# Kernel tuning notes

Measured on AMD Instinct MI355X. Metric: run time of the kernel, lower is better.

Reference implementation:

```python
import jax, jax.numpy as jnp
import numpy as np

N_NODES = 10000
N_EDGES = 640000
D_FEAT = 128


def setup_inputs() -> dict:
    key = jax.random.key(0)
    k1, k2, k3, k4 = jax.random.split(key, 4)
    feat = jax.random.normal(k1, (N_NODES, D_FEAT), dtype=jnp.float32)
    src = jax.random.randint(k2, (N_EDGES,), 0, N_NODES, dtype=jnp.int32)
    dst = jax.random.randint(k3, (N_EDGES,), 0, N_NODES, dtype=jnp.int32)
    W = jax.random.normal(k4, (D_FEAT, D_FEAT), dtype=jnp.float32) / np.sqrt(D_FEAT).astype(np.float32)
    b = jnp.zeros((D_FEAT,), dtype=jnp.float32)
    return {"feat": feat, "W": W, "b": b, "src": src, "dst": dst}


def reference(feat, W, b, src, dst):
    eps = jnp.float32(0.0)  # init_eps=0, learn_eps=False (buffer)
    n = feat.shape[0]
    # message passing: copy_u('h','m') + sum reducer -> neigh[i] = sum_{j->i} h_j
    h_src = feat[src]                                   # [E, D] gather
    neigh = jax.ops.segment_sum(h_src, dst, num_segments=n)  # [N, D] scatter-add
    rst = (1.0 + eps) * feat + neigh
    # apply_func: Linear(D, D)
    rst = rst @ W + b
    # per-edge score: e = sum(h_src * tanh(h_dst), axis=1)
    e = jnp.sum(h_src * jnp.tanh(feat[dst]), axis=1)    # [E]
    # edge_softmax: softmax over edges grouped by destination node
    m = jax.ops.segment_max(e, dst, num_segments=n)     # [N]
    e_exp = jnp.exp(e - m[dst])
    denom = jax.ops.segment_sum(e_exp, dst, num_segments=n)  # [N]
    e_soft = e_exp / denom[dst]
    return rst, e_soft
```

## Files before the change

### kernel.cpp

```cpp
#include <hip/hip_runtime.h>
#include <hip/hip_bf16.h>
#include <math.h>

#define N_NODES 10000
#define N_EDGES 640000
#define D_FEAT  128
#define SLOT    128


__global__ void scatter_build(const int* __restrict__ src,
                              const int* __restrict__ dst,
                              int* __restrict__ cnt,
                              unsigned short* __restrict__ slot_us,
                              int* __restrict__ pos_by_edge) {
    int i = blockIdx.x * 256 + threadIdx.x;
    int d = dst[i];
    int pos = atomicAdd(&cnt[d], 1);
    int idx = d * SLOT + pos;
    slot_us[idx] = (unsigned short)src[i];
    pos_by_edge[i] = idx;
}

__global__ void fused_node(const float* __restrict__ feat,
                           const int* __restrict__ cnt,
                           const unsigned short* __restrict__ slot_us,
                           float* __restrict__ e_slot,
                           float* __restrict__ x_out) {
    __shared__ float t_sh[4][D_FEAT];
    __shared__ float e_sh[4][SLOT];
    int wv = threadIdx.x >> 6;
    int lane = threadIdx.x & 63;
    int node = blockIdx.x * 4 + wv;
    if (node >= N_NODES) return;

    int g = lane >> 4;
    int l = lane & 15;

    int deg = cnt[node];
    unsigned base = (unsigned)node * SLOT;

    float2 fd2 = ((const float2*)(feat + (size_t)node * D_FEAT))[lane];
    ((float2*)&t_sh[wv][0])[lane] = make_float2(tanhf(fd2.x), tanhf(fd2.y));
    float4 t0 = ((const float4*)&t_sh[wv][0])[l * 2];
    float4 t1 = ((const float4*)&t_sh[wv][0])[l * 2 + 1];

    float4 acc0 = make_float4(0.f, 0.f, 0.f, 0.f);
    float4 acc1 = make_float4(0.f, 0.f, 0.f, 0.f);

    for (int cbase = 0; cbase < deg; cbase += 64) {
        int n = min(64, deg - cbase);
        int my_src = (int)slot_us[base + min(cbase + lane, deg - 1)];
        int j = 0;
        for (; j + 8 <= n; j += 8) {
            int s0 = __shfl(my_src, j + g, 64);
            int s1 = __shfl(my_src, j + 4 + g, 64);
            const float4* r0 = (const float4*)(feat + (size_t)s0 * D_FEAT) + l * 2;
            const float4* r1 = (const float4*)(feat + (size_t)s1 * D_FEAT) + l * 2;
            float4 v00 = r0[0], v01 = r0[1];
            float4 v10 = r1[0], v11 = r1[1];
            acc0.x += v00.x + v10.x; acc0.y += v00.y + v10.y;
            acc0.z += v00.z + v10.z; acc0.w += v00.w + v10.w;
            acc1.x += v01.x + v11.x; acc1.y += v01.y + v11.y;
            acc1.z += v01.z + v11.z; acc1.w += v01.w + v11.w;
            float d0 = v00.x * t0.x + v00.y * t0.y + v00.z * t0.z + v00.w * t0.w
                     + v01.x * t1.x + v01.y * t1.y + v01.z * t1.z + v01.w * t1.w;
            float d1 = v10.x * t0.x + v10.y * t0.y + v10.z * t0.z + v10.w * t0.w
                     + v11.x * t1.x + v11.y * t1.y + v11.z * t1.z + v11.w * t1.w;
            #pragma unroll
            for (int off = 1; off <= 8; off <<= 1) {
                d0 += __shfl_xor(d0, off, 64);
                d1 += __shfl_xor(d1, off, 64);
            }
            if (l == 0) {
                e_sh[wv][cbase + j + g] = d0;
                e_sh[wv][cbase + j + 4 + g] = d1;
            }
        }
        for (; j < n; j += 4) {
            int idx = j + g;
            bool act = idx < n;
            int s = __shfl(my_src, min(idx, n - 1), 64);
            const float4* r0 = (const float4*)(feat + (size_t)s * D_FEAT) + l * 2;
            float4 v0 = r0[0], v1 = r0[1];
            if (!act) {
                v0 = make_float4(0.f, 0.f, 0.f, 0.f);
                v1 = make_float4(0.f, 0.f, 0.f, 0.f);
            }
            acc0.x += v0.x; acc0.y += v0.y; acc0.z += v0.z; acc0.w += v0.w;
            acc1.x += v1.x; acc1.y += v1.y; acc1.z += v1.z; acc1.w += v1.w;
            float d = v0.x * t0.x + v0.y * t0.y + v0.z * t0.z + v0.w * t0.w
                    + v1.x * t1.x + v1.y * t1.y + v1.z * t1.z + v1.w * t1.w;
            #pragma unroll
            for (int off = 1; off <= 8; off <<= 1)
                d += __shfl_xor(d, off, 64);
            if (act && l == 0) e_sh[wv][cbase + idx] = d;
        }
    }

    #pragma unroll
    for (int off = 16; off <= 32; off <<= 1) {
        acc0.x += __shfl_xor(acc0.x, off, 64);
        acc0.y += __shfl_xor(acc0.y, off, 64);
        acc0.z += __shfl_xor(acc0.z, off, 64);
        acc0.w += __shfl_xor(acc0.w, off, 64);
        acc1.x += __shfl_xor(acc1.x, off, 64);
        acc1.y += __shfl_xor(acc1.y, off, 64);
        acc1.z += __shfl_xor(acc1.z, off, 64);
        acc1.w += __shfl_xor(acc1.w, off, 64);
    }

    float2 mp = (g == 0) ? make_float2(acc0.x, acc0.y)
              : (g == 1) ? make_float2(acc0.z, acc0.w)
              : (g == 2) ? make_float2(acc1.x, acc1.y)
              :            make_float2(acc1.z, acc1.w);
    int p2 = l * 4 + g;
    float2 fn = ((const float2*)(feat + (size_t)node * D_FEAT))[p2];
    ((float2*)(x_out + (size_t)node * D_FEAT))[p2] =
        make_float2(mp.x + fn.x, mp.y + fn.y);

    float mx = -INFINITY;
    for (int i = lane; i < deg; i += 64) mx = fmaxf(mx, e_sh[wv][i]);
    #pragma unroll
    for (int off = 32; off; off >>= 1)
        mx = fmaxf(mx, __shfl_xor(mx, off, 64));

    float sum = 0.f;
    for (int i = lane; i < deg; i += 64) {
        float ex = expf(e_sh[wv][i] - mx);
        e_sh[wv][i] = ex;
        sum += ex;
    }
    #pragma unroll
    for (int off = 32; off; off >>= 1)
        sum += __shfl_xor(sum, off, 64);

    float inv = 1.0f / sum;
    for (int i = lane; i < deg; i += 64)
        e_slot[base + i] = e_sh[wv][i] * inv;
}

__global__ void gemm_and_edge(float* __restrict__ io,
                              const float* __restrict__ W,
                              const float* __restrict__ b,
                              const int* __restrict__ pos_by_edge,
                              const float* __restrict__ e_slot,
                              float* __restrict__ out_e) {
    if (blockIdx.x >= 625) {
        int i4 = ((blockIdx.x - 625) * 256 + threadIdx.x) * 4;
        int4 p = *(const int4*)&pos_by_edge[i4];
        float4 r;
        r.x = e_slot[p.x];
        r.y = e_slot[p.y];
        r.z = e_slot[p.z];
        r.w = e_slot[p.w];
        *(float4*)&out_e[i4] = r;
        return;
    }

    __shared__ float xst[D_FEAT][20];
    int rbase = blockIdx.x * 16;

    for (int i = threadIdx.x; i < 16 * D_FEAT; i += 256) {
        int r = i >> 7, c = i & 127;
        xst[c][r] = io[(size_t)(rbase + r) * D_FEAT + c];
    }
    __syncthreads();

    int col = threadIdx.x & 127;
    int rh  = threadIdx.x >> 7;
    float acc[8] = {0.f, 0.f, 0.f, 0.f, 0.f, 0.f, 0.f, 0.f};

    for (int k = 0; k < D_FEAT; ++k) {
        float4 xa = *(const float4*)&xst[k][rh * 8];
        float4 xb = *(const float4*)&xst[k][rh * 8 + 4];
        float wk = W[(size_t)k * D_FEAT + col];
        acc[0] += xa.x * wk; acc[1] += xa.y * wk;
        acc[2] += xa.z * wk; acc[3] += xa.w * wk;
        acc[4] += xb.x * wk; acc[5] += xb.y * wk;
        acc[6] += xb.z * wk; acc[7] += xb.w * wk;
    }
    __syncthreads();

    float bias = b[col];
    #pragma unroll
    for (int r = 0; r < 8; ++r)
        io[(size_t)(rbase + rh * 8 + r) * D_FEAT + col] = acc[r] + bias;
}

extern "C" void kernel_launch(void* const* d_in, const int* in_sizes, int n_in,
                              void* d_out, int out_size, void* d_ws, size_t ws_size,
                              hipStream_t stream) {
    const float* feat = (const float*)d_in[0];
    const float* W    = (const float*)d_in[1];
    const float* b    = (const float*)d_in[2];
    const int*   src  = (const int*)d_in[3];
    const int*   dst  = (const int*)d_in[4];

    float* out_rst = (float*)d_out;
    float* out_e   = (float*)d_out + (size_t)N_NODES * D_FEAT;

    char* ws = (char*)d_ws;
    int*            cnt         = (int*)(ws + 0);
    unsigned short* slot_us     = (unsigned short*)(ws + 65536);
    float*          e_slot      = (float*)(ws + 2686976);
    int*            pos_by_edge = (int*)(ws + 7806976);

    hipMemsetAsync(cnt, 0, N_NODES * sizeof(int), stream);

    scatter_build<<<N_EDGES / 256, 256, 0, stream>>>(src, dst, cnt, slot_us, pos_by_edge);

    fused_node<<<(N_NODES + 3) / 4, 256, 0, stream>>>(feat, cnt, slot_us, e_slot, out_rst);

    gemm_and_edge<<<1250, 256, 0, stream>>>(out_rst, W, b, pos_by_edge, e_slot, out_e);
}
```

Baseline: 148.2 us.

## Split per-node edge counters into 8 sub-buckets to reduce atomic contention

Each destination node now has 8 counters and 8 slot segments of 64, chosen by the block index, so atomics in scatter_build land on different addresses. fused_node prefix-sums the 8 counts, compacts the source indices into shared memory, and writes softmax results back to the segmented layout. This targets same-address atomic serialization, at the cost of a larger workspace, a memset eight times bigger, and assumptions that no segment exceeds 64 entries and no node exceeds 128 edges.

```diff
diff --git a/kernel.cpp b/kernel.cpp
--- a/kernel.cpp
+++ b/kernel.cpp
@@ -5,7 +5,9 @@
 #define N_NODES 10000
 #define N_EDGES 640000
 #define D_FEAT  128
-#define SLOT    128
+#define NGRP    8
+#define SEG     64
+#define MAXDEG  128
 
 
 __global__ void scatter_build(const int* __restrict__ src,
@@ -14,9 +16,10 @@
                               unsigned short* __restrict__ slot_us,
                               int* __restrict__ pos_by_edge) {
     int i = blockIdx.x * 256 + threadIdx.x;
+    int g = blockIdx.x & 7;
     int d = dst[i];
-    int pos = atomicAdd(&cnt[d], 1);
-    int idx = d * SLOT + pos;
+    int pos = atomicAdd(&cnt[d * NGRP + g], 1);
+    int idx = d * (NGRP * SEG) + g * SEG + pos;
     slot_us[idx] = (unsigned short)src[i];
     pos_by_edge[i] = idx;
 }
@@ -27,7 +30,8 @@
                            float* __restrict__ e_slot,
                            float* __restrict__ x_out) {
     __shared__ float t_sh[4][D_FEAT];
-    __shared__ float e_sh[4][SLOT];
+    __shared__ float e_sh[4][MAXDEG];
+    __shared__ unsigned short src_sh[4][MAXDEG];
     int wv = threadIdx.x >> 6;
     int lane = threadIdx.x & 63;
     int node = blockIdx.x * 4 + wv;
@@ -36,8 +40,22 @@
     int g = lane >> 4;
     int l = lane & 15;
 
-    int deg = cnt[node];
-    unsigned base = (unsigned)node * SLOT;
+    unsigned sbase = (unsigned)node * (NGRP * SEG);
+
+    int cme = (lane < NGRP) ? cnt[node * NGRP + lane] : 0;
+    int cg[NGRP], psum[NGRP + 1];
+    psum[0] = 0;
+    #pragma unroll
+    for (int k = 0; k < NGRP; ++k) {
+        cg[k] = __shfl(cme, k, 64);
+        psum[k + 1] = psum[k] + cg[k];
+    }
+    int deg = psum[NGRP];
+    #pragma unroll
+    for (int k = 0; k < NGRP; ++k) {
+        if (lane < cg[k])
+            src_sh[wv][psum[k] + lane] = slot_us[sbase + k * SEG + lane];
+    }
 
     float2 fd2 = ((const float2*)(feat + (size_t)node * D_FEAT))[lane];
     ((float2*)&t_sh[wv][0])[lane] = make_float2(tanhf(fd2.x), tanhf(fd2.y));
@@ -49,7 +67,7 @@
 
     for (int cbase = 0; cbase < deg; cbase += 64) {
         int n = min(64, deg - cbase);
-        int my_src = (int)slot_us[base + min(cbase + lane, deg - 1)];
+        int my_src = (int)src_sh[wv][min(cbase + lane, deg - 1)];
         int j = 0;
         for (; j + 8 <= n; j += 8) {
             int s0 = __shfl(my_src, j + g, 64);
@@ -135,8 +153,11 @@
         sum += __shfl_xor(sum, off, 64);
 
     float inv = 1.0f / sum;
-    for (int i = lane; i < deg; i += 64)
-        e_slot[base + i] = e_sh[wv][i] * inv;
+    #pragma unroll
+    for (int k = 0; k < NGRP; ++k) {
+        if (lane < cg[k])
+            e_slot[sbase + k * SEG + lane] = e_sh[wv][psum[k] + lane] * inv;
+    }
 }
 
 __global__ void gemm_and_edge(float* __restrict__ io,
@@ -201,11 +222,11 @@
 
     char* ws = (char*)d_ws;
     int*            cnt         = (int*)(ws + 0);
-    unsigned short* slot_us     = (unsigned short*)(ws + 65536);
-    float*          e_slot      = (float*)(ws + 2686976);
-    int*            pos_by_edge = (int*)(ws + 7806976);
-
-    hipMemsetAsync(cnt, 0, N_NODES * sizeof(int), stream);
+    unsigned short* slot_us     = (unsigned short*)(ws + 320000);
+    float*          e_slot      = (float*)(ws + 10560000);
+    int*            pos_by_edge = (int*)(ws + 31040000);
+
+    hipMemsetAsync(cnt, 0, N_NODES * NGRP * sizeof(int), stream);
 
     scatter_build<<<N_EDGES / 256, 256, 0, stream>>>(src, dst, cnt, slot_us, pos_by_edge);
 
```

Result: faster. 144.7 us (-2.3%).
